# Performance work log

Measured on AMD Instinct MI355X. Metric: run time of the kernel, lower is better.

The kernel has to match this reference:

```python
import jax, jax.numpy as jnp
import numpy as np

D_MODEL = 2048
STATE = 16
KCONV = 4
EXPAND = 2
D_INNER = D_MODEL * EXPAND
EPS = 1e-05


def setup_inputs() -> dict:
    key = jax.random.key(0)
    ks = jax.random.split(key, 10)
    s = 0.02
    x = jax.random.normal(ks[0], (2, 2048, D_MODEL), dtype=jnp.float32)
    norm_w = jnp.ones((D_MODEL,), jnp.float32)
    in_proj_w = jax.random.normal(ks[1], (D_INNER * 2, D_MODEL), jnp.float32) * s
    conv_w = jax.random.normal(ks[2], (D_INNER, 1, KCONV), jnp.float32) * s  # depthwise (O,I/g,K)
    conv_b = jnp.zeros((D_INNER,), jnp.float32)
    x_proj_w = jax.random.normal(ks[3], (STATE * 2 + 1, D_INNER), jnp.float32) * s
    dt_w = jax.random.normal(ks[4], (D_INNER, 1), jnp.float32) * s
    dt_b = jnp.zeros((D_INNER,), jnp.float32)
    A_log = jnp.log(jnp.broadcast_to(jnp.arange(1, STATE + 1, dtype=jnp.float32)[None, :], (D_INNER, STATE)))
    D_param = jnp.ones((D_INNER,), jnp.float32)
    out_proj_w = jax.random.normal(ks[5], (D_MODEL, D_INNER), jnp.float32) * s
    return {"x": x, "norm_w": norm_w, "in_proj_w": in_proj_w, "conv_w": conv_w,
            "conv_b": conv_b, "x_proj_w": x_proj_w, "dt_w": dt_w, "dt_b": dt_b,
            "A_log": A_log, "D_param": D_param, "out_proj_w": out_proj_w}


def _silu(v):
    return v * jax.nn.sigmoid(v)


def reference(x, norm_w, in_proj_w, conv_w, conv_b, x_proj_w, dt_w, dt_b, A_log, D_param, out_proj_w):
    residual = x
    # RMSNorm
    xn = x * jax.lax.rsqrt(jnp.mean(x * x, axis=-1, keepdims=True) + EPS) * norm_w
    # in_proj -> split into x_inner, z
    xz = jnp.einsum('bld,ed->ble', xn, in_proj_w)  # [B,L,2*d_inner]
    x_inner, z = jnp.split(xz, 2, axis=-1)
    # causal depthwise conv1d (torch pads K-1 both sides then truncates to L == left pad only)
    xc = jnp.transpose(x_inner, (0, 2, 1))  # [B,d_inner,L]
    xc = jax.lax.conv_general_dilated(
        xc, conv_w, window_strides=(1,), padding=[(KCONV - 1, 0)],
        dimension_numbers=('NCH', 'OIH', 'NCH'), feature_group_count=D_INNER)
    xc = xc + conv_b[None, :, None]
    xc = _silu(jnp.transpose(xc, (0, 2, 1)))  # [B,L,d_inner]
    # SSM parameter projections
    x_ssm = jnp.einsum('bld,ed->ble', xc, x_proj_w)  # [B,L,2N+1]
    dt = jax.nn.softplus(x_ssm[..., -1:] * dt_w[:, 0] + dt_b)  # [B,L,d_inner]
    B_p = x_ssm[..., :STATE]            # [B,L,N]
    C_p = x_ssm[..., STATE:2 * STATE]   # [B,L,N]
    A = -jnp.exp(A_log)                 # [d_inner,N]

    batch = x.shape[0]
    h0 = jnp.zeros((batch, D_INNER, STATE), x.dtype)

    def step(h, inp):
        dt_t, B_t, C_t, u_t = inp  # [B,d_inner],[B,N],[B,N],[B,d_inner]
        dA = jnp.exp(dt_t[..., None] * A)  # [B,d_inner,N]
        h = dA * h + (dt_t * u_t)[..., None] * B_t[:, None, :]
        y_t = jnp.sum(h * C_t[:, None, :], axis=-1) + D_param * u_t
        return h, y_t

    seq_first = lambda a: jnp.swapaxes(a, 0, 1)
    _, ys = jax.lax.scan(step, h0, (seq_first(dt), seq_first(B_p), seq_first(C_p), seq_first(xc)))
    y = jnp.swapaxes(ys, 0, 1)  # [B,L,d_inner]
    y = y * _silu(z)
    return jnp.einsum('ble,de->bld', y, out_proj_w) + residual
```

## Files before the change

kernel.cpp:

```cpp
#include <hip/hip_runtime.h>

#define NTOK   4096
#define LSEQ   2048
#define DMODEL 2048
#define DINNER 4096
#define NSTATE 16
#define NCHAIN 8192

using short8 = __attribute__((ext_vector_type(8))) short;
using f32x4  = __attribute__((ext_vector_type(4))) float;

__device__ inline float b2f(short s) {
    union { unsigned u; float f; } v;
    v.u = ((unsigned)(unsigned short)s) << 16;
    return v.f;
}
__device__ inline short f2b(float f) {
    unsigned u = __float_as_uint(f);
    unsigned r = (u + 0x7fffu + ((u >> 16) & 1u)) >> 16;
    return (short)r;
}

__global__ __launch_bounds__(256) void f32_to_bf16_kernel(
    const float* __restrict__ in, short* __restrict__ out, int n8) {
    int i = blockIdx.x * 256 + threadIdx.x;
    if (i >= n8) return;
    const float4* p = (const float4*)in + 2 * (size_t)i;
    float4 a = p[0], b = p[1];
    short8 s;
    s[0] = f2b(a.x); s[1] = f2b(a.y); s[2] = f2b(a.z); s[3] = f2b(a.w);
    s[4] = f2b(b.x); s[5] = f2b(b.y); s[6] = f2b(b.z); s[7] = f2b(b.w);
    *(short8*)(out + 8 * (size_t)i) = s;
}

__global__ __launch_bounds__(256) void rmsnorm_kernel(
    const float* __restrict__ x, const float* __restrict__ w,
    short* __restrict__ xn) {
    const int t = blockIdx.x, tid = threadIdx.x;
    const float4* xr = (const float4*)(x + (size_t)t * DMODEL + tid * 8);
    float4 a = xr[0], b = xr[1];
    float v[8] = {a.x, a.y, a.z, a.w, b.x, b.y, b.z, b.w};
    float ss = 0.f;
#pragma unroll
    for (int j = 0; j < 8; ++j) ss += v[j] * v[j];
#pragma unroll
    for (int o = 32; o > 0; o >>= 1) ss += __shfl_down(ss, o, 64);
    __shared__ float sred[4];
    if ((tid & 63) == 0) sred[tid >> 6] = ss;
    __syncthreads();
    float r = rsqrtf((sred[0] + sred[1] + sred[2] + sred[3]) * (1.f / DMODEL) + 1e-5f);
    const float4* wr = (const float4*)(w + tid * 8);
    float4 wa = wr[0], wb = wr[1];
    float wv[8] = {wa.x, wa.y, wa.z, wa.w, wb.x, wb.y, wb.z, wb.w};
    short8 o8;
#pragma unroll
    for (int j = 0; j < 8; ++j) o8[j] = f2b(v[j] * r * wv[j]);
    *(short8*)(xn + (size_t)t * DMODEL + tid * 8) = o8;
}

template <bool ADD_RES, bool F32OUT, bool SPLIT>
__global__ __launch_bounds__(256) void gemm_bt(
    const short* __restrict__ A, const short* __restrict__ B,
    const float* __restrict__ RES, void* __restrict__ Cp, void* __restrict__ Cp2,
    int M, int N, int K) {
    __shared__ __align__(16) short As[128 * 32];
    __shared__ __align__(16) short Bs[128 * 32];

    const int tid  = threadIdx.x;
    const int wave = tid >> 6;
    const int lane = tid & 63;
    const int lr   = lane & 15;
    const int q    = lane >> 4;
    const int m0   = blockIdx.x * 128;
    const int n0   = blockIdx.y * 128;
    const int wm   = (wave >> 1) * 64;
    const int wn   = (wave & 1) * 64;

    f32x4 acc[4][4] = {};

    for (int k0 = 0; k0 < K; k0 += 32) {
#pragma unroll
        for (int p = 0; p < 2; ++p) {
            int i16 = p * 256 + tid;
            int row = i16 >> 2, ch = i16 & 3;
            const short* ga = A + (size_t)(m0 + row) * K + k0 + ch * 8;
            const short* gb = B + (size_t)(n0 + row) * K + k0 + ch * 8;
            __builtin_amdgcn_global_load_lds(
                (const __attribute__((address_space(1))) void*)ga,
                (__attribute__((address_space(3))) void*)((char*)As + i16 * 16),
                16, 0, 0);
            __builtin_amdgcn_global_load_lds(
                (const __attribute__((address_space(1))) void*)gb,
                (__attribute__((address_space(3))) void*)((char*)Bs + i16 * 16),
                16, 0, 0);
        }
        __syncthreads();

        short8 af[4], bfr[4];
#pragma unroll
        for (int i = 0; i < 4; ++i) {
            af[i]  = *(const short8*)&As[(wm + i * 16 + lr) * 32 + q * 8];
            bfr[i] = *(const short8*)&Bs[(wn + i * 16 + lr) * 32 + q * 8];
        }
#pragma unroll
        for (int i = 0; i < 4; ++i)
#pragma unroll
            for (int j = 0; j < 4; ++j)
                acc[i][j] = __builtin_amdgcn_mfma_f32_16x16x32_bf16(
                    af[i], bfr[j], acc[i][j], 0, 0, 0);
        __syncthreads();
    }

    short* sdst = nullptr;
    int    noff = 0;
    if (SPLIT) {
        bool hi = (n0 >= DINNER);
        sdst = hi ? (short*)Cp2 : (short*)Cp;
        noff = hi ? DINNER : 0;
    }

#pragma unroll
    for (int i = 0; i < 4; ++i)
#pragma unroll
        for (int j = 0; j < 4; ++j)
#pragma unroll
            for (int r = 0; r < 4; ++r) {
                int m = m0 + wm + i * 16 + q * 4 + r;
                int n = n0 + wn + j * 16 + lr;
                float v = acc[i][j][r];
                if (SPLIT) {
                    sdst[(size_t)m * DINNER + (n - noff)] = f2b(v);
                } else {
                    size_t idx = (size_t)m * N + n;
                    if (ADD_RES) v += RES[idx];
                    if (F32OUT) ((float*)Cp)[idx] = v;
                    else        ((short*)Cp)[idx] = f2b(v);
                }
            }
}

__global__ __launch_bounds__(256) void conv_silu_kernel(
    const short* __restrict__ xi, const float* __restrict__ cw,
    const float* __restrict__ cb, short* __restrict__ xc) {
    const int t = blockIdx.x;
    const int b = t >> 11, l = t & 2047;
    for (int c = threadIdx.x; c < DINNER; c += 256) {
        float acc = cb[c];
#pragma unroll
        for (int k = 0; k < 4; ++k) {
            int ls = l - 3 + k;
            if (ls >= 0)
                acc += b2f(xi[(size_t)(b * LSEQ + ls) * DINNER + c]) *
                       cw[c * 4 + k];
        }
        xc[(size_t)t * DINNER + c] = f2b(acc / (1.f + __expf(-acc)));
    }
}

__global__ __launch_bounds__(256) void xproj_kernel(
    const short* __restrict__ xc, const float* __restrict__ W,
    float* __restrict__ BT, float* __restrict__ CT, float* __restrict__ s32T) {
    const int t = blockIdx.x, tid = threadIdx.x;
    float xv[16];
    {
        short8 a = *(const short8*)(xc + (size_t)t * DINNER + tid * 16);
        short8 b = *(const short8*)(xc + (size_t)t * DINNER + tid * 16 + 8);
#pragma unroll
        for (int j = 0; j < 8; ++j) { xv[j] = b2f(a[j]); xv[8 + j] = b2f(b[j]); }
    }
    float acc[33];
#pragma unroll
    for (int e = 0; e < 33; ++e) {
        const float4* wr = (const float4*)(W + (size_t)e * DINNER + tid * 16);
        float4 w0 = wr[0], w1 = wr[1], w2 = wr[2], w3 = wr[3];
        float wv[16] = {w0.x, w0.y, w0.z, w0.w, w1.x, w1.y, w1.z, w1.w,
                        w2.x, w2.y, w2.z, w2.w, w3.x, w3.y, w3.z, w3.w};
        float s = 0.f;
#pragma unroll
        for (int j = 0; j < 16; ++j) s += xv[j] * wv[j];
        acc[e] = s;
    }
    __shared__ float red[4][33];
#pragma unroll
    for (int e = 0; e < 33; ++e) {
        float v = acc[e];
#pragma unroll
        for (int o = 32; o > 0; o >>= 1) v += __shfl_down(v, o, 64);
        if ((tid & 63) == 0) red[tid >> 6][e] = v;
    }
    __syncthreads();
    if (tid < 33) {
        float val = red[0][tid] + red[1][tid] + red[2][tid] + red[3][tid];
        const int bb = t >> 11, l = t & (LSEQ - 1);
        if (tid < 16)
            BT[((size_t)bb * NSTATE + tid) * LSEQ + l] = val;
        else if (tid < 32)
            CT[((size_t)bb * NSTATE + (tid - 16)) * LSEQ + l] = val;
        else
            s32T[(size_t)bb * LSEQ + l] = val;
    }
}

__global__ __launch_bounds__(256) void transpose_xc_kernel(
    const short* __restrict__ xc, short* __restrict__ uT) {
    __shared__ short tile[64][66];
    const int bb = blockIdx.z;
    const int l0 = blockIdx.x * 64;
    const int c0 = blockIdx.y * 64;
    const int tid = threadIdx.x;
    const int rr = tid >> 3;
    const int c8 = (tid & 7) * 8;
#pragma unroll
    for (int p = 0; p < 2; ++p) {
        int r = p * 32 + rr;
        short8 v = *(const short8*)(xc + ((size_t)(bb * LSEQ + l0 + r)) * DINNER + c0 + c8);
#pragma unroll
        for (int j = 0; j < 8; ++j) tile[r][c8 + j] = v[j];
    }
    __syncthreads();
#pragma unroll
    for (int p = 0; p < 2; ++p) {
        int cr = p * 32 + rr;
        short8 v;
#pragma unroll
        for (int j = 0; j < 8; ++j) v[j] = tile[c8 + j][cr];
        *(short8*)(uT + ((size_t)(bb * DINNER + c0 + cr)) * LSEQ + l0 + c8) = v;
    }
}

__global__ __launch_bounds__(256) void dt_kernel(
    const float* __restrict__ s32T, const float* __restrict__ dt_w,
    const float* __restrict__ dt_b, float* __restrict__ dtT0,
    float* __restrict__ dtT1) {
    const int chain = blockIdx.x;
    const int b = chain >> 12;
    const int c = chain & (DINNER - 1);
    const float dtw = dt_w[c], dtb = dt_b[c];
    const float* src = s32T + (size_t)b * LSEQ + threadIdx.x * 8;
    float* dst = (b ? dtT1 : dtT0) + (size_t)c * LSEQ + threadIdx.x * 8;
    float4 s0 = ((const float4*)src)[0], s1 = ((const float4*)src)[1];
    float sv[8] = {s0.x, s0.y, s0.z, s0.w, s1.x, s1.y, s1.z, s1.w};
    float dv[8];
#pragma unroll
    for (int j = 0; j < 8; ++j) {
        float v = sv[j] * dtw + dtb;
        dv[j] = (v > 20.f) ? v : __logf(1.f + __expf(v));
    }
    ((float4*)dst)[0] = make_float4(dv[0], dv[1], dv[2], dv[3]);
    ((float4*)dst)[1] = make_float4(dv[4], dv[5], dv[6], dv[7]);
}

#define GQ 4
__global__ __launch_bounds__(256) void scan_state_kernel(
    const float* __restrict__ BT, const float* __restrict__ CT,
    const float* __restrict__ dtT0, const float* __restrict__ dtT1,
    const short* __restrict__ uT, const short* __restrict__ Z,
    short* __restrict__ yout,
    const float* __restrict__ A_log, const float* __restrict__ D_par) {
    const int tid   = threadIdx.x;
    const int n     = tid & 15;
    const int chain = blockIdx.x * 16 + (tid >> 4);
    const int b     = chain >> 12;
    const int c     = chain & (DINNER - 1);

    const float An = -__expf(A_log[c * NSTATE + n]);
    const float Dp = D_par[c];

    const float* Bb = BT + ((size_t)b * NSTATE + n) * LSEQ;
    const float* Cb = CT + ((size_t)b * NSTATE + n) * LSEQ;
    const float* db = (b ? dtT1 : dtT0) + (size_t)c * LSEQ;
    const short* ub = uT + (size_t)chain * LSEQ;
    const short* ue = ub + n;
    const short* zp = Z + ((size_t)b * LSEQ + n) * DINNER + c;
    short*       yp = yout + ((size_t)b * LSEQ + n) * DINNER + c;

    f32x4 Bq[GQ], Cq[GQ], dq[GQ];
    uint2 uq[GQ];
#pragma unroll
    for (int g = 0; g < GQ; ++g) {
        Bq[g] = *(const f32x4*)(Bb + g * 4);
        Cq[g] = *(const f32x4*)(Cb + g * 4);
        dq[g] = *(const f32x4*)(db + g * 4);
        uq[g] = *(const uint2*)(ub + g * 4);
    }

    float h = 0.f;
    for (int l0 = 0; l0 < LSEQ; l0 += 16) {
        const float u_n = b2f(ue[0]);
        const float z_n = b2f(zp[0]);
        float ys = 0.f;
#pragma unroll
        for (int g = 0; g < GQ; ++g) {
            f32x4 B4 = Bq[g], C4 = Cq[g], d4 = dq[g];
            uint2 u4 = uq[g];
            int lp  = l0 + 16 + g * 4;
            int lpc = (lp > LSEQ - 4) ? (LSEQ - 4) : lp;
            Bq[g] = *(const f32x4*)(Bb + lpc);
            Cq[g] = *(const f32x4*)(Cb + lpc);
            dq[g] = *(const f32x4*)(db + lpc);
            uq[g] = *(const uint2*)(ub + lpc);
#pragma unroll
            for (int i = 0; i < 4; ++i) {
                const float Bv = B4[i], Cv = C4[i], dt = d4[i];
                float u;
                {
                    unsigned uw = (i < 2) ? u4.x : u4.y;
                    union { unsigned uu; float ff; } t;
                    t.uu = (i & 1) ? (uw & 0xffff0000u) : (uw << 16);
                    u = t.ff;
                }
                h = __expf(dt * An) * h + (dt * u) * Bv;
                float part = h * Cv;
#pragma unroll
                for (int o = 8; o > 0; o >>= 1) part += __shfl_xor(part, o, 16);
                ys = (n == g * 4 + i) ? part : ys;
            }
        }
        float y  = ys + Dp * u_n;
        float zg = z_n / (1.f + __expf(-z_n));
        yp[0] = f2b(y * zg);
        ue += 16;
        zp += (size_t)16 * DINNER;
        yp += (size_t)16 * DINNER;
    }
}

extern "C" void kernel_launch(void* const* d_in, const int* in_sizes, int n_in,
                              void* d_out, int out_size, void* d_ws, size_t ws_size,
                              hipStream_t stream) {
    const float* x      = (const float*)d_in[0];
    const float* norm_w = (const float*)d_in[1];
    const float* w_in   = (const float*)d_in[2];
    const float* conv_w = (const float*)d_in[3];
    const float* conv_b = (const float*)d_in[4];
    const float* w_xp   = (const float*)d_in[5];
    const float* dt_w   = (const float*)d_in[6];
    const float* dt_b   = (const float*)d_in[7];
    const float* A_log  = (const float*)d_in[8];
    const float* D_par  = (const float*)d_in[9];
    const float* w_out  = (const float*)d_in[10];
    float* out = (float*)d_out;

    char* ws = (char*)d_ws;
    short* wb   = (short*)(ws);
    short* xn   = (short*)(ws + (size_t)(32 << 20));
    short* Xi   = (short*)(ws + (size_t)(48 << 20));
    short* Zb   = (short*)(ws + (size_t)(80 << 20));
    short* xc   = (short*)(ws + (size_t)(112 << 20));
    float* BT   = (float*)(ws + (size_t)(144 << 20));
    float* CT   = (float*)(ws + (size_t)(144 << 20) + (256 << 10));
    float* s32T = (float*)(ws + (size_t)(144 << 20) + (512 << 10));
    float* dtT0 = (float*)Xi;
    float* dtT1 = out;

    f32_to_bf16_kernel<<<(2 * DINNER * DMODEL / 8) / 256, 256, 0, stream>>>(
        w_in, wb, 2 * DINNER * DMODEL / 8);
    rmsnorm_kernel<<<NTOK, 256, 0, stream>>>(x, norm_w, xn);
    gemm_bt<false, false, true><<<dim3(NTOK / 128, 8192 / 128), 256, 0, stream>>>(
        xn, wb, nullptr, Xi, Zb, NTOK, 2 * DINNER, DMODEL);
    conv_silu_kernel<<<NTOK, 256, 0, stream>>>(Xi, conv_w, conv_b, xc);
    xproj_kernel<<<NTOK, 256, 0, stream>>>(xc, w_xp, BT, CT, s32T);
    transpose_xc_kernel<<<dim3(LSEQ / 64, DINNER / 64, 2), 256, 0, stream>>>(
        xc, wb);
    dt_kernel<<<NCHAIN, 256, 0, stream>>>(s32T, dt_w, dt_b, dtT0, dtT1);
    scan_state_kernel<<<NCHAIN / 16, 256, 0, stream>>>(
        BT, CT, dtT0, dtT1, wb, Zb, xc, A_log, D_par);
    f32_to_bf16_kernel<<<(DMODEL * DINNER / 8) / 256, 256, 0, stream>>>(
        w_out, xn, DMODEL * DINNER / 8);
    gemm_bt<true, true, false><<<dim3(NTOK / 128, DMODEL / 128), 256, 0, stream>>>(
        xc, xn, x, out, nullptr, NTOK, DMODEL, DINNER);
}
```

Before: 1.151 ms.

## Fuse conv+SiLU with transpose, batch xproj tokens, use DPP reductions in scan

Merges the depthwise conv+SiLU kernel with the xc transpose, so each 64x64 tile is convolved from shared memory and written both row-major and transposed. This drops the separate transpose kernel and its re-read of xc. The xproj kernel now handles two tokens per block so each weight load is reused twice. The scan kernel batches four timesteps' exps and replaces shfl_xor reductions with ds_swizzle and DPP quad permutes to shorten its critical latency chain.

```diff
diff --git a/kernel.cpp b/kernel.cpp
--- a/kernel.cpp
+++ b/kernel.cpp
@@ -19,6 +19,16 @@
     unsigned u = __float_as_uint(f);
     unsigned r = (u + 0x7fffu + ((u >> 16) & 1u)) >> 16;
     return (short)r;
+}
+
+template <int OFF>
+__device__ inline float swz(float v) {
+    return __int_as_float(__builtin_amdgcn_ds_swizzle(__float_as_int(v), OFF));
+}
+template <int CTRL>
+__device__ inline float qperm(float v) {
+    return __int_as_float(
+        __builtin_amdgcn_mov_dpp(__float_as_int(v), CTRL, 0xF, 0xF, true));
 }
 
 __global__ __launch_bounds__(256) void f32_to_bf16_kernel(
@@ -139,92 +149,126 @@
             }
 }
 
-__global__ __launch_bounds__(256) void conv_silu_kernel(
+__global__ __launch_bounds__(256) void conv_silu_t_kernel(
     const short* __restrict__ xi, const float* __restrict__ cw,
-    const float* __restrict__ cb, short* __restrict__ xc) {
-    const int t = blockIdx.x;
-    const int b = t >> 11, l = t & 2047;
-    for (int c = threadIdx.x; c < DINNER; c += 256) {
+    const float* __restrict__ cb, short* __restrict__ xc,
+    short* __restrict__ uT) {
+    __shared__ short tin[67][72];
+    __shared__ short tout[64][72];
+    const int bb = blockIdx.z;
+    const int l0 = blockIdx.x * 64;
+    const int c0 = blockIdx.y * 64;
+    const int tid = threadIdx.x;
+
+    for (int idx = tid; idx < 67 * 8; idx += 256) {
+        int row = idx >> 3, cs = (idx & 7) * 8;
+        int ls = l0 - 3 + row;
+        short8 v;
+        if (ls >= 0) {
+            v = *(const short8*)(xi + ((size_t)(bb * LSEQ + ls)) * DINNER + c0 + cs);
+        } else {
+#pragma unroll
+            for (int j = 0; j < 8; ++j) v[j] = 0;
+        }
+        *(short8*)&tin[row][cs] = v;
+    }
+    __syncthreads();
+
+    const int r   = tid >> 2;
+    const int cb16 = (tid & 3) * 16;
+    short8 a[4][2];
+#pragma unroll
+    for (int k = 0; k < 4; ++k) {
+        a[k][0] = *(const short8*)&tin[r + k][cb16];
+        a[k][1] = *(const short8*)&tin[r + k][cb16 + 8];
+    }
+    short o16[16];
+#pragma unroll
+    for (int j = 0; j < 16; ++j) {
+        const int c = c0 + cb16 + j;
+        float4 w4 = *(const float4*)(cw + (size_t)c * 4);
         float acc = cb[c];
-#pragma unroll
-        for (int k = 0; k < 4; ++k) {
-            int ls = l - 3 + k;
-            if (ls >= 0)
-                acc += b2f(xi[(size_t)(b * LSEQ + ls) * DINNER + c]) *
-                       cw[c * 4 + k];
-        }
-        xc[(size_t)t * DINNER + c] = f2b(acc / (1.f + __expf(-acc)));
+        acc += b2f(a[0][j >> 3][j & 7]) * w4.x;
+        acc += b2f(a[1][j >> 3][j & 7]) * w4.y;
+        acc += b2f(a[2][j >> 3][j & 7]) * w4.z;
+        acc += b2f(a[3][j >> 3][j & 7]) * w4.w;
+        o16[j] = f2b(acc / (1.f + __expf(-acc)));
+    }
+    {
+        short8 lo, hi;
+#pragma unroll
+        for (int j = 0; j < 8; ++j) { lo[j] = o16[j]; hi[j] = o16[8 + j]; }
+        short* dst = xc + ((size_t)(bb * LSEQ + l0 + r)) * DINNER + c0 + cb16;
+        *(short8*)dst = lo;
+        *(short8*)(dst + 8) = hi;
+    }
+#pragma unroll
+    for (int j = 0; j < 16; ++j) tout[r][cb16 + j] = o16[j];
+    __syncthreads();
+
+    const int rr = tid >> 3;
+    const int l8 = (tid & 7) * 8;
+#pragma unroll
+    for (int p = 0; p < 2; ++p) {
+        int cr = p * 32 + rr;
+        short8 v;
+#pragma unroll
+        for (int j = 0; j < 8; ++j) v[j] = tout[l8 + j][cr];
+        *(short8*)(uT + ((size_t)(bb * DINNER + c0 + cr)) * LSEQ + l0 + l8) = v;
     }
 }
 
 __global__ __launch_bounds__(256) void xproj_kernel(
     const short* __restrict__ xc, const float* __restrict__ W,
     float* __restrict__ BT, float* __restrict__ CT, float* __restrict__ s32T) {
-    const int t = blockIdx.x, tid = threadIdx.x;
-    float xv[16];
+    const int t0 = blockIdx.x * 2, tid = threadIdx.x;
+    float xv0[16], xv1[16];
     {
-        short8 a = *(const short8*)(xc + (size_t)t * DINNER + tid * 16);
-        short8 b = *(const short8*)(xc + (size_t)t * DINNER + tid * 16 + 8);
-#pragma unroll
-        for (int j = 0; j < 8; ++j) { xv[j] = b2f(a[j]); xv[8 + j] = b2f(b[j]); }
-    }
-    float acc[33];
+        short8 a = *(const short8*)(xc + (size_t)t0 * DINNER + tid * 16);
+        short8 b = *(const short8*)(xc + (size_t)t0 * DINNER + tid * 16 + 8);
+        short8 c = *(const short8*)(xc + (size_t)(t0 + 1) * DINNER + tid * 16);
+        short8 d = *(const short8*)(xc + (size_t)(t0 + 1) * DINNER + tid * 16 + 8);
+#pragma unroll
+        for (int j = 0; j < 8; ++j) {
+            xv0[j] = b2f(a[j]); xv0[8 + j] = b2f(b[j]);
+            xv1[j] = b2f(c[j]); xv1[8 + j] = b2f(d[j]);
+        }
+    }
+    float acc0[33], acc1[33];
 #pragma unroll
     for (int e = 0; e < 33; ++e) {
         const float4* wr = (const float4*)(W + (size_t)e * DINNER + tid * 16);
         float4 w0 = wr[0], w1 = wr[1], w2 = wr[2], w3 = wr[3];
         float wv[16] = {w0.x, w0.y, w0.z, w0.w, w1.x, w1.y, w1.z, w1.w,
                         w2.x, w2.y, w2.z, w2.w, w3.x, w3.y, w3.z, w3.w};
-        float s = 0.f;
-#pragma unroll
-        for (int j = 0; j < 16; ++j) s += xv[j] * wv[j];
-        acc[e] = s;
+        float s0 = 0.f, s1 = 0.f;
+#pragma unroll
+        for (int j = 0; j < 16; ++j) { s0 += xv0[j] * wv[j]; s1 += xv1[j] * wv[j]; }
+        acc0[e] = s0; acc1[e] = s1;
     }
     __shared__ float red[4][33];
 #pragma unroll
-    for (int e = 0; e < 33; ++e) {
-        float v = acc[e];
-#pragma unroll
-        for (int o = 32; o > 0; o >>= 1) v += __shfl_down(v, o, 64);
-        if ((tid & 63) == 0) red[tid >> 6][e] = v;
-    }
-    __syncthreads();
-    if (tid < 33) {
-        float val = red[0][tid] + red[1][tid] + red[2][tid] + red[3][tid];
-        const int bb = t >> 11, l = t & (LSEQ - 1);
-        if (tid < 16)
-            BT[((size_t)bb * NSTATE + tid) * LSEQ + l] = val;
-        else if (tid < 32)
-            CT[((size_t)bb * NSTATE + (tid - 16)) * LSEQ + l] = val;
-        else
-            s32T[(size_t)bb * LSEQ + l] = val;
-    }
-}
-
-__global__ __launch_bounds__(256) void transpose_xc_kernel(
-    const short* __restrict__ xc, short* __restrict__ uT) {
-    __shared__ short tile[64][66];
-    const int bb = blockIdx.z;
-    const int l0 = blockIdx.x * 64;
-    const int c0 = blockIdx.y * 64;
-    const int tid = threadIdx.x;
-    const int rr = tid >> 3;
-    const int c8 = (tid & 7) * 8;
-#pragma unroll
-    for (int p = 0; p < 2; ++p) {
-        int r = p * 32 + rr;
-        short8 v = *(const short8*)(xc + ((size_t)(bb * LSEQ + l0 + r)) * DINNER + c0 + c8);
-#pragma unroll
-        for (int j = 0; j < 8; ++j) tile[r][c8 + j] = v[j];
-    }
-    __syncthreads();
-#pragma unroll
-    for (int p = 0; p < 2; ++p) {
-        int cr = p * 32 + rr;
-        short8 v;
-#pragma unroll
-        for (int j = 0; j < 8; ++j) v[j] = tile[c8 + j][cr];
-        *(short8*)(uT + ((size_t)(bb * DINNER + c0 + cr)) * LSEQ + l0 + c8) = v;
+    for (int tk = 0; tk < 2; ++tk) {
+#pragma unroll
+        for (int e = 0; e < 33; ++e) {
+            float v = tk ? acc1[e] : acc0[e];
+#pragma unroll
+            for (int o = 32; o > 0; o >>= 1) v += __shfl_down(v, o, 64);
+            if ((tid & 63) == 0) red[tid >> 6][e] = v;
+        }
+        __syncthreads();
+        if (tid < 33) {
+            float val = red[0][tid] + red[1][tid] + red[2][tid] + red[3][tid];
+            const int t = t0 + tk;
+            const int bb = t >> 11, l = t & (LSEQ - 1);
+            if (tid < 16)
+                BT[((size_t)bb * NSTATE + tid) * LSEQ + l] = val;
+            else if (tid < 32)
+                CT[((size_t)bb * NSTATE + (tid - 16)) * LSEQ + l] = val;
+            else
+                s32T[(size_t)bb * LSEQ + l] = val;
+        }
+        __syncthreads();
     }
 }
 
@@ -299,22 +343,37 @@
             Cq[g] = *(const f32x4*)(Cb + lpc);
             dq[g] = *(const f32x4*)(db + lpc);
             uq[g] = *(const uint2*)(ub + lpc);
+
+            float uv[4], e[4];
 #pragma unroll
             for (int i = 0; i < 4; ++i) {
-                const float Bv = B4[i], Cv = C4[i], dt = d4[i];
-                float u;
-                {
-                    unsigned uw = (i < 2) ? u4.x : u4.y;
-                    union { unsigned uu; float ff; } t;
-                    t.uu = (i & 1) ? (uw & 0xffff0000u) : (uw << 16);
-                    u = t.ff;
-                }
-                h = __expf(dt * An) * h + (dt * u) * Bv;
-                float part = h * Cv;
-#pragma unroll
-                for (int o = 8; o > 0; o >>= 1) part += __shfl_xor(part, o, 16);
-                ys = (n == g * 4 + i) ? part : ys;
+                unsigned uw = (i < 2) ? u4.x : u4.y;
+                union { unsigned uu; float ff; } t;
+                t.uu = (i & 1) ? (uw & 0xffff0000u) : (uw << 16);
+                uv[i] = t.ff;
+                e[i]  = __expf(d4[i] * An);
             }
+            float part[4];
+#pragma unroll
+            for (int i = 0; i < 4; ++i) {
+                h = e[i] * h + (d4[i] * uv[i]) * B4[i];
+                part[i] = h * C4[i];
+            }
+            float tmp[4];
+#pragma unroll
+            for (int i = 0; i < 4; ++i) tmp[i] = swz<0x201F>(part[i]);
+#pragma unroll
+            for (int i = 0; i < 4; ++i) part[i] += tmp[i];
+#pragma unroll
+            for (int i = 0; i < 4; ++i) tmp[i] = swz<0x101F>(part[i]);
+#pragma unroll
+            for (int i = 0; i < 4; ++i) part[i] += tmp[i];
+#pragma unroll
+            for (int i = 0; i < 4; ++i) part[i] += qperm<0x4E>(part[i]);
+#pragma unroll
+            for (int i = 0; i < 4; ++i) part[i] += qperm<0xB1>(part[i]);
+#pragma unroll
+            for (int i = 0; i < 4; ++i) ys = (n == g * 4 + i) ? part[i] : ys;
         }
         float y  = ys + Dp * u_n;
         float zg = z_n / (1.f + __expf(-z_n));
@@ -358,10 +417,9 @@
     rmsnorm_kernel<<<NTOK, 256, 0, stream>>>(x, norm_w, xn);
     gemm_bt<false, false, true><<<dim3(NTOK / 128, 8192 / 128), 256, 0, stream>>>(
         xn, wb, nullptr, Xi, Zb, NTOK, 2 * DINNER, DMODEL);
-    conv_silu_kernel<<<NTOK, 256, 0, stream>>>(Xi, conv_w, conv_b, xc);
-    xproj_kernel<<<NTOK, 256, 0, stream>>>(xc, w_xp, BT, CT, s32T);
-    transpose_xc_kernel<<<dim3(LSEQ / 64, DINNER / 64, 2), 256, 0, stream>>>(
-        xc, wb);
+    conv_silu_t_kernel<<<dim3(LSEQ / 64, DINNER / 64, 2), 256, 0, stream>>>(
+        Xi, conv_w, conv_b, xc, wb);
+    xproj_kernel<<<NTOK / 2, 256, 0, stream>>>(xc, w_xp, BT, CT, s32T);
     dt_kernel<<<NCHAIN, 256, 0, stream>>>(s32T, dt_w, dt_b, dtT0, dtT1);
     scan_state_kernel<<<NCHAIN / 16, 256, 0, stream>>>(
         BT, CT, dtT0, dtT1, wb, Zb, xc, A_log, D_par);
```

Measured after the change: 1.080 ms. 6.1% less time.
